# Optimization experiments

Measured on AMD Instinct MI355X. Metric: run time of the kernel, lower is better.

The kernel has to match this reference:

```python
import jax, jax.numpy as jnp
import numpy as np

B, T, D = 32, 2048, 512


def setup_inputs() -> dict:
    key = jax.random.key(0)
    x = jax.random.normal(key, (B, T, D), dtype=jnp.float32)
    return {"x": x}


def reference(x):
    """DmvCell RNN with aggregations ('mean','var','max').

    Active partials: count, sum, max, mean, sn (Welford M2), var.
    Per step t:
        count += 1
        sum   += x_t
        max    = maximum(max, x_t)
        prev_mean = mean; mean = sum / count
        sn    += (x_t - prev_mean) * (x_t - mean)
        var    = sn / count
        out_t  = concat([mean, var, max])
    Initial states are zeros (Keras default). Returns the full output
    sequence [B, T, 3*D].
    """
    b, t, d = x.shape
    dt = x.dtype

    def step(carry, xt):
        count, s, mx, mean, sn = carry
        count = count + jnp.asarray(1, dt)          # [B,1]
        s = s + xt                                   # [B,D]
        mx = jnp.maximum(mx, xt)                     # [B,D]
        prev_mean = mean
        mean = s / count                             # [B,D]
        sn = sn + (xt - prev_mean) * (xt - mean)     # [B,D]
        var = sn / count                             # [B,D]
        out = jnp.concatenate([mean, var, mx], axis=-1)  # [B,3D]
        return (count, s, mx, mean, sn), out

    init = (
        jnp.zeros((b, 1), dt),   # count
        jnp.zeros((b, d), dt),   # sum
        jnp.zeros((b, d), dt),   # max
        jnp.zeros((b, d), dt),   # mean
        jnp.zeros((b, d), dt),   # sn
    )
    _, ys = jax.lax.scan(step, init, jnp.swapaxes(x, 0, 1))  # ys: [T,B,3D]
    return jnp.swapaxes(ys, 0, 1)  # [B,T,3D]
```

## Files before the change

kernel.cpp:

```cpp
#include <hip/hip_runtime.h>


#define BB 32
#define TT 2048
#define DD 512
#define NCHAIN (BB * DD)
#define NF4PERB 128

typedef float f32x4 __attribute__((ext_vector_type(4)));

__device__ __forceinline__ float fast_rcp(float x) {
#if __has_builtin(__builtin_amdgcn_rcpf)
    return __builtin_amdgcn_rcpf(x);
#else
    return 1.0f / x;
#endif
}

__device__ __forceinline__ f32x4 vmax4(f32x4 a, f32x4 b) {
#if __has_builtin(__builtin_elementwise_max)
    return __builtin_elementwise_max(a, b);
#else
    f32x4 r;
    r.x = fmaxf(a.x, b.x); r.y = fmaxf(a.y, b.y);
    r.z = fmaxf(a.z, b.z); r.w = fmaxf(a.w, b.w);
    return r;
#endif
}

__device__ __forceinline__ void nts(f32x4 v, float* p) {
#if __has_builtin(__builtin_nontemporal_store)
    __builtin_nontemporal_store(v, (f32x4*)p);
#else
    *(f32x4*)p = v;
#endif
}

template <int NC>
__launch_bounds__(256)
__global__ void dmv_agg_kernel(const float* __restrict__ x,
                               f32x4* __restrict__ ws4) {
    constexpr int CHUNK = TT / NC;
    f32x4* __restrict__ aS  = ws4;
    f32x4* __restrict__ aM2 = ws4 + (size_t)NC * 4096;
    f32x4* __restrict__ aMX = ws4 + 2 * (size_t)NC * 4096;

    const int tid = blockIdx.x * 256 + threadIdx.x;
    const int W   = tid >> 6;
    const int l   = tid & 63;
    const int c   = W & (NC - 1);
    const int b   = W / NC;

    const float* xp = x + ((size_t)(b * TT + c * CHUNK)) * DD + 4 * l;

    f32x4 s0 = {0,0,0,0}, s1 = {0,0,0,0};
    f32x4 q0 = {0,0,0,0}, q1 = {0,0,0,0};
    f32x4 m0 = {0,0,0,0}, m1 = {0,0,0,0};
    #pragma unroll 4
    for (int k = 0; k < CHUNK; ++k) {
        f32x4 a = *(const f32x4*)(xp + (size_t)k * DD);
        f32x4 b2 = *(const f32x4*)(xp + (size_t)k * DD + 256);
        s0 += a;  q0 += a * a;   m0 = vmax4(m0, a);
        s1 += b2; q1 += b2 * b2; m1 = vmax4(m1, b2);
    }
    const size_t o = (size_t)c * 4096 + (size_t)b * NF4PERB + l;
    const float ic = 1.0f / (float)CHUNK;
    aS[o]       = s0;  aS[o + 64]  = s1;
    aM2[o]      = q0 - s0 * s0 * ic;
    aM2[o + 64] = q1 - s1 * s1 * ic;
    aMX[o]      = m0;  aMX[o + 64] = m1;
}

template <int NC>
__launch_bounds__(256)
__global__ void dmv_prefix_kernel(float* __restrict__ ws) {
    constexpr int CHUNK = TT / NC;
    float* __restrict__ aS  = ws;
    float* __restrict__ aM2 = ws + (size_t)NC * NCHAIN;
    float* __restrict__ aMX = ws + 2 * (size_t)NC * NCHAIN;

    const int i = blockIdx.x * 256 + threadIdx.x;

    float rs = aS[i], rm2 = aM2[i], rmx = aMX[i];
    aS[i] = 0.f; aM2[i] = 0.f; aMX[i] = 0.f;
    float rn = (float)CHUNK;
    #pragma unroll 8
    for (int c = 1; c < NC; ++c) {
        const size_t idx = (size_t)c * NCHAIN + i;
        float ts = aS[idx], tm2 = aM2[idx], tmx = aMX[idx];
        aS[idx] = rs; aM2[idx] = rm2; aMX[idx] = rmx;
        float n  = rn + (float)CHUNK;
        float da = ts * (1.f / CHUNK) - rs / rn;
        rm2 = rm2 + tm2 + da * da * (rn * (float)CHUNK / n);
        rs += ts;
        rmx = fmaxf(rmx, tmx);
        rn  = n;
    }
}

template <int NC>
__launch_bounds__(256)
__global__ void dmv_scan_kernel3(const float* __restrict__ x,
                                 const f32x4* __restrict__ ws4,
                                 float* __restrict__ out) {
    constexpr int CHUNK = TT / NC;
    const f32x4* __restrict__ aS  = ws4;
    const f32x4* __restrict__ aM2 = ws4 + (size_t)NC * 4096;
    const f32x4* __restrict__ aMX = ws4 + 2 * (size_t)NC * 4096;

    const int tid = blockIdx.x * 256 + threadIdx.x;
    const int W   = tid >> 6;
    const int l   = tid & 63;
    const int c   = W & (NC - 1);
    const int b   = W / NC;

    const size_t o = (size_t)c * 4096 + (size_t)b * NF4PERB + l;
    f32x4 rs0 = aS[o],  rs1 = aS[o + 64];
    f32x4 rm20 = aM2[o], rm21 = aM2[o + 64];
    f32x4 rmx0 = aMX[o], rmx1 = aMX[o + 64];

    float cnt = (float)(c * CHUNK);
    f32x4 rmean0 = {0,0,0,0}, rmean1 = {0,0,0,0};
    if (c > 0) {
        float icnt = fast_rcp(cnt);
        rmean0 = rs0 * icnt;
        rmean1 = rs1 * icnt;
    }

    const float* xp = x   + ((size_t)(b * TT + c * CHUNK)) * DD + 4 * l;
    float*       op = out + ((size_t)(b * TT + c * CHUNK)) * (3 * DD) + 4 * l;

    #pragma unroll 4
    for (int k = 0; k < CHUNK; ++k) {
        f32x4 v0 = *(const f32x4*)(xp + (size_t)k * DD);
        f32x4 v1 = *(const f32x4*)(xp + (size_t)k * DD + 256);
        cnt += 1.f;
        float inv = fast_rcp(cnt);
        rs0 += v0; rs1 += v1;
        rmx0 = vmax4(rmx0, v0); rmx1 = vmax4(rmx1, v1);
        f32x4 nm0 = rs0 * inv, nm1 = rs1 * inv;
        rm20 += (v0 - rmean0) * (v0 - nm0);
        rm21 += (v1 - rmean1) * (v1 - nm1);
        rmean0 = nm0; rmean1 = nm1;
        f32x4 var0 = rm20 * inv, var1 = rm21 * inv;
        float* row = op + (size_t)k * (3 * DD);
        nts(nm0,  row);        nts(nm1,  row + 256);
        nts(var0, row + 512);  nts(var1, row + 768);
        nts(rmx0, row + 1024); nts(rmx1, row + 1280);
    }
}

#define FNW 16
#define FCHUNK (TT / FNW)
#define DGRP 64

__launch_bounds__(1024, 1)
__global__ void dmv_scan_fallback(const float* __restrict__ x,
                                  float* __restrict__ out) {
    __shared__ float aggS[FNW][DGRP];
    __shared__ float aggM2[FNW][DGRP];
    __shared__ float aggMX[FNW][DGRP];

    const int tid = threadIdx.x;
    const int w   = tid >> 6;
    const int l   = tid & 63;
    const int b   = blockIdx.x >> 3;
    const int d0  = (blockIdx.x & 7) * DGRP;

    const float* xp = x   + ((size_t)b * TT) * DD + d0 + l
                          + (size_t)(w * FCHUNK) * DD;
    float*       op = out + ((size_t)b * TT) * (3 * DD) + d0 + l
                          + (size_t)(w * FCHUNK) * (3 * DD);

    if (w < FNW - 1) {
        float s = 0.f, ss = 0.f, mx = 0.f;
        #pragma unroll 8
        for (int k = 0; k < FCHUNK; ++k) {
            float xv = xp[(size_t)k * DD];
            s += xv; ss = fmaf(xv, xv, ss); mx = fmaxf(mx, xv);
        }
        aggS[w][l] = s;
        aggM2[w][l] = ss - s * s * (1.0f / FCHUNK);
        aggMX[w][l] = mx;
    }
    __syncthreads();

    float c_n = 0.f, c_s = 0.f, c_m2 = 0.f, c_mx = 0.f;
    for (int j = 0; j < w; ++j) {
        float bs = aggS[j][l], bm2 = aggM2[j][l], bmx = aggMX[j][l];
        if (j == 0) {
            c_n = (float)FCHUNK; c_s = bs; c_m2 = bm2; c_mx = bmx;
        } else {
            float n  = c_n + (float)FCHUNK;
            float da = bs * (1.0f / FCHUNK) - c_s / c_n;
            c_m2 = c_m2 + bm2 + da * da * (c_n * (float)FCHUNK / n);
            c_s += bs; c_mx = fmaxf(c_mx, bmx); c_n = n;
        }
    }

    float cnt = c_n, rs = c_s, rm2 = c_m2, rmx = c_mx;
    float rmean = (w > 0) ? rs / cnt : 0.f;
    #pragma unroll 8
    for (int k = 0; k < FCHUNK; ++k) {
        float xv = xp[(size_t)k * DD];
        cnt += 1.f;
        float inv = fast_rcp(cnt);
        rs += xv; rmx = fmaxf(rmx, xv);
        float nm = rs * inv;
        rm2 += (xv - rmean) * (xv - nm);
        rmean = nm;
        float var = rm2 * inv;
        float* orow = op + (size_t)k * (3 * DD);
        orow[0] = nm; orow[DD] = var; orow[2 * DD] = rmx;
    }
}

template <int NC>
static void launch_3k(const float* x, float* out, void* d_ws, hipStream_t stream) {
    dim3 blk(256);
    dmv_agg_kernel<NC><<<dim3(8 * NC), blk, 0, stream>>>(x, (f32x4*)d_ws);
    dmv_prefix_kernel<NC><<<dim3(NCHAIN / 256), blk, 0, stream>>>((float*)d_ws);
    dmv_scan_kernel3<NC><<<dim3(8 * NC), blk, 0, stream>>>(x, (const f32x4*)d_ws, out);
}

extern "C" void kernel_launch(void* const* d_in, const int* in_sizes, int n_in,
                              void* d_out, int out_size, void* d_ws, size_t ws_size,
                              hipStream_t stream) {
    (void)in_sizes; (void)n_in; (void)out_size;
    const float* x = (const float*)d_in[0];
    float* out = (float*)d_out;

    const size_t need128 = (size_t)3 * 128 * NCHAIN * sizeof(float);
    const size_t need64  = (size_t)3 * 64  * NCHAIN * sizeof(float);
    const size_t need32  = (size_t)3 * 32  * NCHAIN * sizeof(float);

    if (d_ws && ws_size >= need128) {
        launch_3k<128>(x, out, d_ws, stream);
    } else if (d_ws && ws_size >= need64) {
        launch_3k<64>(x, out, d_ws, stream);
    } else if (d_ws && ws_size >= need32) {
        launch_3k<32>(x, out, d_ws, stream);
    } else {
        dmv_scan_fallback<<<dim3(BB * (DD / DGRP)), dim3(1024), 0, stream>>>(x, out);
    }
}
```

Measured before the change: 133.5 us.

## Fuse chunk prefix combine into scan kernel, drop separate prefix launch

Removes the standalone prefix kernel. Each scan wave now combines the aggregates of all earlier chunks itself, using a Chan-style merge of sum, M2 and max, before running its local scan. This saves one kernel launch and the read-modify-write pass over the workspace, in exchange for redundant O(c) combine work per wave. The chunk count is also capped at 64 instead of 128, so the chunks are longer and the redundant prefix work stays bounded.

```diff
diff --git a/kernel.cpp b/kernel.cpp
--- a/kernel.cpp
+++ b/kernel.cpp
@@ -58,7 +58,7 @@
     f32x4 m0 = {0,0,0,0}, m1 = {0,0,0,0};
     #pragma unroll 4
     for (int k = 0; k < CHUNK; ++k) {
-        f32x4 a = *(const f32x4*)(xp + (size_t)k * DD);
+        f32x4 a  = *(const f32x4*)(xp + (size_t)k * DD);
         f32x4 b2 = *(const f32x4*)(xp + (size_t)k * DD + 256);
         s0 += a;  q0 += a * a;   m0 = vmax4(m0, a);
         s1 += b2; q1 += b2 * b2; m1 = vmax4(m1, b2);
@@ -73,36 +73,9 @@
 
 template <int NC>
 __launch_bounds__(256)
-__global__ void dmv_prefix_kernel(float* __restrict__ ws) {
-    constexpr int CHUNK = TT / NC;
-    float* __restrict__ aS  = ws;
-    float* __restrict__ aM2 = ws + (size_t)NC * NCHAIN;
-    float* __restrict__ aMX = ws + 2 * (size_t)NC * NCHAIN;
-
-    const int i = blockIdx.x * 256 + threadIdx.x;
-
-    float rs = aS[i], rm2 = aM2[i], rmx = aMX[i];
-    aS[i] = 0.f; aM2[i] = 0.f; aMX[i] = 0.f;
-    float rn = (float)CHUNK;
-    #pragma unroll 8
-    for (int c = 1; c < NC; ++c) {
-        const size_t idx = (size_t)c * NCHAIN + i;
-        float ts = aS[idx], tm2 = aM2[idx], tmx = aMX[idx];
-        aS[idx] = rs; aM2[idx] = rm2; aMX[idx] = rmx;
-        float n  = rn + (float)CHUNK;
-        float da = ts * (1.f / CHUNK) - rs / rn;
-        rm2 = rm2 + tm2 + da * da * (rn * (float)CHUNK / n);
-        rs += ts;
-        rmx = fmaxf(rmx, tmx);
-        rn  = n;
-    }
-}
-
-template <int NC>
-__launch_bounds__(256)
-__global__ void dmv_scan_kernel3(const float* __restrict__ x,
-                                 const f32x4* __restrict__ ws4,
-                                 float* __restrict__ out) {
+__global__ void dmv_scan_fused(const float* __restrict__ x,
+                               const f32x4* __restrict__ ws4,
+                               float* __restrict__ out) {
     constexpr int CHUNK = TT / NC;
     const f32x4* __restrict__ aS  = ws4;
     const f32x4* __restrict__ aM2 = ws4 + (size_t)NC * 4096;
@@ -114,12 +87,35 @@
     const int c   = W & (NC - 1);
     const int b   = W / NC;
 
-    const size_t o = (size_t)c * 4096 + (size_t)b * NF4PERB + l;
-    f32x4 rs0 = aS[o],  rs1 = aS[o + 64];
-    f32x4 rm20 = aM2[o], rm21 = aM2[o + 64];
-    f32x4 rmx0 = aMX[o], rmx1 = aMX[o + 64];
-
-    float cnt = (float)(c * CHUNK);
+    f32x4 rs0 = {0,0,0,0}, rs1 = {0,0,0,0};
+    f32x4 rm20 = {0,0,0,0}, rm21 = {0,0,0,0};
+    f32x4 rmx0 = {0,0,0,0}, rmx1 = {0,0,0,0};
+    float rn = 0.f;
+    if (c > 0) {
+        const size_t o0 = (size_t)b * NF4PERB + l;
+        rs0  = aS[o0];  rs1  = aS[o0 + 64];
+        rm20 = aM2[o0]; rm21 = aM2[o0 + 64];
+        rmx0 = aMX[o0]; rmx1 = aMX[o0 + 64];
+        rn = (float)CHUNK;
+        for (int j = 1; j < c; ++j) {
+            const size_t oj = (size_t)j * 4096 + (size_t)b * NF4PERB + l;
+            f32x4 ts0 = aS[oj],  ts1 = aS[oj + 64];
+            f32x4 tm0 = aM2[oj], tm1 = aM2[oj + 64];
+            f32x4 tx0 = aMX[oj], tx1 = aMX[oj + 64];
+            float n     = rn + (float)CHUNK;
+            float irn   = fast_rcp(rn);
+            float scale = rn * (float)CHUNK * fast_rcp(n);
+            f32x4 da0 = ts0 * (1.0f / CHUNK) - rs0 * irn;
+            f32x4 da1 = ts1 * (1.0f / CHUNK) - rs1 * irn;
+            rm20 += tm0 + da0 * da0 * scale;
+            rm21 += tm1 + da1 * da1 * scale;
+            rs0 += ts0; rs1 += ts1;
+            rmx0 = vmax4(rmx0, tx0); rmx1 = vmax4(rmx1, tx1);
+            rn = n;
+        }
+    }
+
+    float cnt = rn;
     f32x4 rmean0 = {0,0,0,0}, rmean1 = {0,0,0,0};
     if (c > 0) {
         float icnt = fast_rcp(cnt);
@@ -216,11 +212,10 @@
 }
 
 template <int NC>
-static void launch_3k(const float* x, float* out, void* d_ws, hipStream_t stream) {
+static void launch_2k(const float* x, float* out, void* d_ws, hipStream_t stream) {
     dim3 blk(256);
     dmv_agg_kernel<NC><<<dim3(8 * NC), blk, 0, stream>>>(x, (f32x4*)d_ws);
-    dmv_prefix_kernel<NC><<<dim3(NCHAIN / 256), blk, 0, stream>>>((float*)d_ws);
-    dmv_scan_kernel3<NC><<<dim3(8 * NC), blk, 0, stream>>>(x, (const f32x4*)d_ws, out);
+    dmv_scan_fused<NC><<<dim3(8 * NC), blk, 0, stream>>>(x, (const f32x4*)d_ws, out);
 }
 
 extern "C" void kernel_launch(void* const* d_in, const int* in_sizes, int n_in,
@@ -230,16 +225,13 @@
     const float* x = (const float*)d_in[0];
     float* out = (float*)d_out;
 
-    const size_t need128 = (size_t)3 * 128 * NCHAIN * sizeof(float);
-    const size_t need64  = (size_t)3 * 64  * NCHAIN * sizeof(float);
-    const size_t need32  = (size_t)3 * 32  * NCHAIN * sizeof(float);
-
-    if (d_ws && ws_size >= need128) {
-        launch_3k<128>(x, out, d_ws, stream);
-    } else if (d_ws && ws_size >= need64) {
-        launch_3k<64>(x, out, d_ws, stream);
+    const size_t need64 = (size_t)3 * 64 * NCHAIN * sizeof(float);
+    const size_t need32 = (size_t)3 * 32 * NCHAIN * sizeof(float);
+
+    if (d_ws && ws_size >= need64) {
+        launch_2k<64>(x, out, d_ws, stream);
     } else if (d_ws && ws_size >= need32) {
-        launch_3k<32>(x, out, d_ws, stream);
+        launch_2k<32>(x, out, d_ws, stream);
     } else {
         dmv_scan_fallback<<<dim3(BB * (DD / DGRP)), dim3(1024), 0, stream>>>(x, out);
     }
```

Result: faster. 121.8 us (-8.7%).
